# Kernel tuning notes

Measured on AMD Instinct MI355X. Metric: run time of the kernel, lower is better.

The kernel has to match this reference:

```python
import jax, jax.numpy as jnp
import numpy as np

DEPTH, FEAT, HID = 20, 2048, 1024
HALF = FEAT // 2
CLAMP = 2.0
TWO_OVER_PI = 0.6366197723675814  # FrEIA's 0.636619772


def setup_inputs() -> dict:
    key = jax.random.key(0)
    ks = jax.random.split(key, 9)
    x = jax.random.normal(ks[0], (4096, FEAT), dtype=jnp.float32)
    # FrEIA PermuteRandom: numpy permutation seeded with layer index k
    perms = jnp.asarray(
        np.stack([np.random.RandomState(k).permutation(FEAT) for k in range(DEPTH)]),
        dtype=jnp.int32,
    )
    def w(k, shape):  # module reinits all params as 0.01*randn
        return 0.01 * jax.random.normal(k, shape, dtype=jnp.float32)
    return {
        "x": x, "perms": perms,
        "s1_w1": w(ks[1], (DEPTH, HALF, HID)), "s1_b1": w(ks[2], (DEPTH, HID)),
        "s1_w2": w(ks[3], (DEPTH, HID, FEAT)), "s1_b2": w(ks[4], (DEPTH, FEAT)),
        "s2_w1": w(ks[5], (DEPTH, HALF, HID)), "s2_b1": w(ks[6], (DEPTH, HID)),
        "s2_w2": w(ks[7], (DEPTH, HID, FEAT)), "s2_b2": w(ks[8], (DEPTH, FEAT)),
    }


def _subnet(x, w1, b1, w2, b2):
    h = x @ w1 + b1
    h = jnp.where(h >= 0, h, 0.01 * h)  # LeakyReLU(negative_slope=0.01)
    return h @ w2 + b2


def reference(x, perms, s1_w1, s1_b1, s1_w2, s1_b2, s2_w1, s2_b1, s2_w2, s2_b2):
    def body(carry, xs):
        z, jac = carry
        perm, w1a, b1a, w1b, b1b, w2a, b2a, w2b, b2b = xs
        z = z[:, perm]                       # PermuteRandom
        x1, x2 = z[:, :HALF], z[:, HALF:]    # GLOW coupling split
        r2 = _subnet(x2, w2a, b2a, w2b, b2b)  # [B, FEAT] -> (s2, t2)
        e2 = CLAMP * TWO_OVER_PI * jnp.arctan(r2[:, :HALF] / CLAMP)
        y1 = jnp.exp(e2) * x1 + r2[:, HALF:]
        r1 = _subnet(y1, w1a, b1a, w1b, b1b)  # (s1, t1)
        e1 = CLAMP * TWO_OVER_PI * jnp.arctan(r1[:, :HALF] / CLAMP)
        y2 = jnp.exp(e1) * x2 + r1[:, HALF:]
        jac = jac + e1.sum(-1) + e2.sum(-1)  # log|det J| per sample
        return (jnp.concatenate([y1, y2], axis=-1), jac), None

    jac0 = jnp.zeros(x.shape[0], dtype=x.dtype)
    (z, jac), _ = jax.lax.scan(
        body, (x, jac0),
        (perms, s1_w1, s1_b1, s1_w2, s1_b2, s2_w1, s2_b1, s2_w2, s2_b2),
    )
    return z, jac
```

## Files before the change

kernel.cpp:

```cpp
#include <hip/hip_runtime.h>
#include <stdint.h>

#define DEPTH 20
#define FEAT  2048
#define HALF  1024
#define HID   1024
#define MROWS 4096

typedef __bf16 bf16x8 __attribute__((ext_vector_type(8)));
typedef float  f32x4  __attribute__((ext_vector_type(4)));
typedef unsigned int u32x4 __attribute__((ext_vector_type(4)));

__device__ __forceinline__ unsigned short f2bf(float f) {
  union { float f; unsigned int u; } v; v.f = f;
  unsigned int u = v.u + 0x7fffu + ((v.u >> 16) & 1u);
  return (unsigned short)(u >> 16);
}

__device__ __forceinline__ void async_cp16(unsigned short* lds, const unsigned short* g) {
  __builtin_amdgcn_global_load_lds(
      (const __attribute__((address_space(1))) void*)g,
      (__attribute__((address_space(3))) void*)lds, 16, 0, 0);
}

__device__ __forceinline__ bf16x8 lds_ld8(const unsigned short* p) {
  return __builtin_bit_cast(bf16x8, *(const u32x4*)p);
}

__global__ void wcvt_k(const float* __restrict__ s2w1, const float* __restrict__ s2w2,
                       const float* __restrict__ s1w1, const float* __restrict__ s1w2,
                       unsigned short* __restrict__ w2a, unsigned short* __restrict__ w2b,
                       unsigned short* __restrict__ w1a, unsigned short* __restrict__ w1b) {
  const float* src; unsigned short* dst; int N, pp;
  switch (blockIdx.z) {
    case 0:  src = s2w1; dst = w2a; N = 1024; pp = 0; break;
    case 1:  src = s2w2; dst = w2b; N = 2048; pp = 1; break;
    case 2:  src = s1w1; dst = w1a; N = 1024; pp = 0; break;
    default: src = s1w2; dst = w1b; N = 2048; pp = 1; break;
  }
  int nb = blockIdx.x * 32;
  if (nb >= N) return;
  int kb = blockIdx.y * 32;
  __shared__ float t[32][33];
  int tx = threadIdx.x, ty = threadIdx.y;
#pragma unroll
  for (int s = 0; s < 4; ++s)
    t[ty + 8*s][tx] = src[(size_t)(kb + ty + 8*s) * N + nb + tx];
  __syncthreads();
  int pbase = pp ? (nb < 1024 ? 2*nb : 2*(nb - 1024) + 32) : nb;
#pragma unroll
  for (int s = 0; s < 4; ++s) {
    int nl = ty + 8*s;
    dst[(size_t)(pbase + nl) * 1024 + kb + tx] = f2bf(t[tx][nl]);
  }
}

__device__ __forceinline__ int porig(int p) {
  int g = p >> 6, o = p & 63;
  return (o < 32) ? (g*32 + o) : (1024 + g*32 + (o - 32));
}

__global__ void bias_k(const float* __restrict__ s2b1, const float* __restrict__ s2b2,
                       const float* __restrict__ s1b1, const float* __restrict__ s1b2,
                       float* __restrict__ b2a, float* __restrict__ b2b,
                       float* __restrict__ b1a, float* __restrict__ b1b) {
  int i = blockIdx.x * 256 + threadIdx.x;
  if (i < 1024)      b2a[i] = s2b1[i];
  else if (i < 3072) { int p = i - 1024; b2b[p] = s2b2[porig(p)]; }
  else if (i < 4096) b1a[i - 3072] = s1b1[i - 3072];
  else               { int p = i - 4096; b1b[p] = s1b2[porig(p)]; }
}

__global__ void permute_k(const float* __restrict__ z, const int* __restrict__ perm,
                          float* __restrict__ x1f, float* __restrict__ x2f,
                          unsigned short* __restrict__ x2b) {
  int c = blockIdx.x * 256 + threadIdx.x;
  int row0 = blockIdx.y * 8;
  int pc = perm[c];
#pragma unroll
  for (int r = 0; r < 8; ++r) {
    int row = row0 + r;
    float v = z[row * FEAT + pc];
    if (c < HALF) {
      x1f[row * HALF + c] = v;
    } else {
      x2f[row * HALF + c - HALF] = v;
      x2b[row * HALF + c - HALF] = f2bf(v);
    }
  }
}

template<int EPI>
__launch_bounds__(256)
__global__ void gemm_k(const unsigned short* __restrict__ A,
                       const unsigned short* __restrict__ Bt,
                       const float* __restrict__ bias,
                       const float* __restrict__ xin,
                       float* __restrict__ yout,
                       unsigned short* __restrict__ ybf,
                       float* __restrict__ jac,
                       unsigned short* __restrict__ hout) {
  __shared__ unsigned short As[128 * 32];
  __shared__ unsigned short Bs[128 * 32];
  const int tid  = threadIdx.x;
  const int wave = tid >> 6, lane = tid & 63;
  const int quad = lane >> 4, l15 = lane & 15;
  const int wy = wave >> 1, wx = wave & 1;
  const int bm = blockIdx.y * 128;
  const int bn = blockIdx.x * 128;
  const int K = 1024;

  f32x4 acc[4][4];
#pragma unroll
  for (int i = 0; i < 4; ++i)
#pragma unroll
    for (int j = 0; j < 4; ++j)
#pragma unroll
      for (int r = 0; r < 4; ++r) acc[i][j][r] = 0.0f;

  const int gbase = wave * 64 + lane;

  for (int kt = 0; kt < 32; ++kt) {
    const int k0 = kt * 32;
#pragma unroll
    for (int i = 0; i < 2; ++i) {
      int g  = i * 256 + gbase;
      int r  = g >> 2, kg = g & 3;
      async_cp16(&As[(i * 256 + wave * 64) * 8], A  + (size_t)(bm + r) * K + k0 + kg * 8);
      async_cp16(&Bs[(i * 256 + wave * 64) * 8], Bt + (size_t)(bn + r) * K + k0 + kg * 8);
    }
    asm volatile("s_waitcnt vmcnt(0)" ::: "memory");
    __syncthreads();

    bf16x8 af[4], bf[4];
#pragma unroll
    for (int i = 0; i < 4; ++i)
      af[i] = lds_ld8(&As[(wy * 64 + i * 16 + l15) * 32 + quad * 8]);
#pragma unroll
    for (int j = 0; j < 4; ++j)
      bf[j] = lds_ld8(&Bs[(wx * 64 + j * 16 + l15) * 32 + quad * 8]);
#pragma unroll
    for (int i = 0; i < 4; ++i)
#pragma unroll
      for (int j = 0; j < 4; ++j)
        acc[i][j] = __builtin_amdgcn_mfma_f32_16x16x32_bf16(af[i], bf[j], acc[i][j], 0, 0, 0);
    __syncthreads();
  }

  if (EPI == 0) {
    const int ldo = gridDim.x * 128;
#pragma unroll
    for (int j = 0; j < 4; ++j) {
      int col = bn + wx * 64 + j * 16 + l15;
      float bj = bias[col];
#pragma unroll
      for (int i = 0; i < 4; ++i) {
#pragma unroll
        for (int r = 0; r < 4; ++r) {
          int row = bm + wy * 64 + i * 16 + quad * 4 + r;
          float v = acc[i][j][r] + bj;
          v = v >= 0.0f ? v : 0.01f * v;
          hout[(size_t)row * ldo + col] = f2bf(v);
        }
      }
    }
  } else {
    const int g = (bn >> 6) + wx;
#pragma unroll
    for (int i = 0; i < 4; ++i) {
      float esum[4] = {0.0f, 0.0f, 0.0f, 0.0f};
#pragma unroll
      for (int j = 0; j < 2; ++j) {
        int pe = bn + wx * 64 + j * 16 + l15;
        float be = bias[pe];
        float ba = bias[pe + 32];
        int xcol = g * 32 + j * 16 + l15;
#pragma unroll
        for (int r = 0; r < 4; ++r) {
          int row = bm + wy * 64 + i * 16 + quad * 4 + r;
          float re = acc[i][j][r] + be;
          float ra = acc[i][j + 2][r] + ba;
          float e  = 1.2732395447351628f * atanf(0.5f * re);
          float y  = __expf(e) * xin[(size_t)row * HALF + xcol] + ra;
          yout[(size_t)row * FEAT + xcol] = y;
          if (ybf) ybf[(size_t)row * HALF + xcol] = f2bf(y);
          esum[r] += e;
        }
      }
#pragma unroll
      for (int r = 0; r < 4; ++r) {
        float v = esum[r];
        v += __shfl_xor(v, 1);
        v += __shfl_xor(v, 2);
        v += __shfl_xor(v, 4);
        v += __shfl_xor(v, 8);
        if (l15 == 0) {
          int row = bm + wy * 64 + i * 16 + quad * 4 + r;
          atomicAdd(&jac[row], v);
        }
      }
    }
  }
}

__global__ void jcopy_k(const float* __restrict__ jac, float* __restrict__ out) {
  int i = blockIdx.x * 256 + threadIdx.x;
  if (i < 4096) out[i] = jac[i];
}

extern "C" void kernel_launch(void* const* d_in, const int* in_sizes, int n_in,
                              void* d_out, int out_size, void* d_ws, size_t ws_size,
                              hipStream_t stream) {
  const float* x     = (const float*)d_in[0];
  const int*   perms = (const int*)d_in[1];
  const float* s1w1  = (const float*)d_in[2];
  const float* s1b1  = (const float*)d_in[3];
  const float* s1w2  = (const float*)d_in[4];
  const float* s1b2  = (const float*)d_in[5];
  const float* s2w1  = (const float*)d_in[6];
  const float* s2b1  = (const float*)d_in[7];
  const float* s2w2  = (const float*)d_in[8];
  const float* s2b2  = (const float*)d_in[9];
  float* out = (float*)d_out;

  size_t off = 0;
  char* base = (char*)d_ws;
  auto alloc = [&](size_t bytes) {
    void* r = base + off;
    off += (bytes + 255) & ~(size_t)255;
    return r;
  };
  float*          x1f = (float*)alloc((size_t)MROWS * HALF * 4);
  float*          x2f = (float*)alloc((size_t)MROWS * HALF * 4);
  unsigned short* x2b = (unsigned short*)alloc((size_t)MROWS * HALF * 2);
  unsigned short* y1b = (unsigned short*)alloc((size_t)MROWS * HALF * 2);
  unsigned short* hb  = (unsigned short*)alloc((size_t)MROWS * HID * 2);
  float*          zbuf= (float*)alloc((size_t)MROWS * FEAT * 4);
  unsigned short* w2a = (unsigned short*)alloc((size_t)HALF * HID * 2);
  unsigned short* w2b = (unsigned short*)alloc((size_t)FEAT * HID * 2);
  unsigned short* w1a = (unsigned short*)alloc((size_t)HALF * HID * 2);
  unsigned short* w1b = (unsigned short*)alloc((size_t)FEAT * HID * 2);
  float* b2a = (float*)alloc(1024 * 4);
  float* b2b = (float*)alloc(2048 * 4);
  float* b1a = (float*)alloc(1024 * 4);
  float* b1b = (float*)alloc(2048 * 4);
  float* jac = (float*)alloc(4096 * 4);

  hipMemsetAsync(jac, 0, 4096 * 4, stream);

  for (int d = 0; d < DEPTH; ++d) {
    wcvt_k<<<dim3(64, 32, 4), dim3(32, 8), 0, stream>>>(
        s2w1 + (size_t)d * HALF * HID, s2w2 + (size_t)d * HID * FEAT,
        s1w1 + (size_t)d * HALF * HID, s1w2 + (size_t)d * HID * FEAT,
        w2a, w2b, w1a, w1b);
    bias_k<<<24, 256, 0, stream>>>(s2b1 + (size_t)d * HID, s2b2 + (size_t)d * FEAT,
                                   s1b1 + (size_t)d * HID, s1b2 + (size_t)d * FEAT,
                                   b2a, b2b, b1a, b1b);
    const float* zsrc = (d == 0) ? x : zbuf;
    permute_k<<<dim3(8, 512), 256, 0, stream>>>(zsrc, perms + (size_t)d * FEAT, x1f, x2f, x2b);

    float* zdst = (d == DEPTH - 1) ? out : zbuf;
    gemm_k<0><<<dim3(8, 32), 256, 0, stream>>>(x2b, w2a, b2a, nullptr, nullptr, nullptr, nullptr, hb);
    gemm_k<1><<<dim3(16, 32), 256, 0, stream>>>(hb, w2b, b2b, x1f, zdst, y1b, jac, nullptr);
    gemm_k<0><<<dim3(8, 32), 256, 0, stream>>>(y1b, w1a, b1a, nullptr, nullptr, nullptr, nullptr, hb);
    gemm_k<1><<<dim3(16, 32), 256, 0, stream>>>(hb, w1b, b1b, x2f, zdst + HALF, nullptr, jac, nullptr);
  }
  jcopy_k<<<16, 256, 0, stream>>>(jac, out + (size_t)MROWS * FEAT);
}
```

Measured before the change: 3.763 ms.

## Triple-buffer GEMM LDS tiles and hoist weight conversion out of layer loop

The GEMM main loop now uses three LDS buffers with asynchronous global-to-LDS loads issued two k-tiles ahead, waiting only on older loads via partial vmcnt counts. This overlaps memory latency with MFMA work where the old loop serialized load, wait, and compute. Separately, weight transposition/bf16 conversion and bias reordering for all layers are done in one batched launch before the loop, removing 40 small launches. The cost is three times the LDS per block, which may reduce occupancy, plus more workspace for all-layer bf16 weights.

```diff
diff --git a/kernel.cpp b/kernel.cpp
--- a/kernel.cpp
+++ b/kernel.cpp
@@ -27,16 +27,24 @@
   return __builtin_bit_cast(bf16x8, *(const u32x4*)p);
 }
 
+__device__ __forceinline__ void wg_barrier() {
+  asm volatile("" ::: "memory");
+  __builtin_amdgcn_s_barrier();
+  asm volatile("" ::: "memory");
+}
+
 __global__ void wcvt_k(const float* __restrict__ s2w1, const float* __restrict__ s2w2,
                        const float* __restrict__ s1w1, const float* __restrict__ s1w2,
                        unsigned short* __restrict__ w2a, unsigned short* __restrict__ w2b,
                        unsigned short* __restrict__ w1a, unsigned short* __restrict__ w1b) {
+  const int zid = blockIdx.z;
+  const int d = zid >> 2, which = zid & 3;
   const float* src; unsigned short* dst; int N, pp;
-  switch (blockIdx.z) {
-    case 0:  src = s2w1; dst = w2a; N = 1024; pp = 0; break;
-    case 1:  src = s2w2; dst = w2b; N = 2048; pp = 1; break;
-    case 2:  src = s1w1; dst = w1a; N = 1024; pp = 0; break;
-    default: src = s1w2; dst = w1b; N = 2048; pp = 1; break;
+  switch (which) {
+    case 0:  src = s2w1 + (size_t)d * HALF * HID;  dst = w2a + (size_t)d * HALF * HID; N = 1024; pp = 0; break;
+    case 1:  src = s2w2 + (size_t)d * HID * FEAT;  dst = w2b + (size_t)d * FEAT * HID; N = 2048; pp = 1; break;
+    case 2:  src = s1w1 + (size_t)d * HALF * HID;  dst = w1a + (size_t)d * HALF * HID; N = 1024; pp = 0; break;
+    default: src = s1w2 + (size_t)d * HID * FEAT;  dst = w1b + (size_t)d * FEAT * HID; N = 2048; pp = 1; break;
   }
   int nb = blockIdx.x * 32;
   if (nb >= N) return;
@@ -65,10 +73,12 @@
                        float* __restrict__ b2a, float* __restrict__ b2b,
                        float* __restrict__ b1a, float* __restrict__ b1b) {
   int i = blockIdx.x * 256 + threadIdx.x;
-  if (i < 1024)      b2a[i] = s2b1[i];
-  else if (i < 3072) { int p = i - 1024; b2b[p] = s2b2[porig(p)]; }
-  else if (i < 4096) b1a[i - 3072] = s1b1[i - 3072];
-  else               { int p = i - 4096; b1b[p] = s1b2[porig(p)]; }
+  if (i >= DEPTH * 6144) return;
+  int d = i / 6144, j = i - d * 6144;
+  if (j < 1024)      b2a[d*1024 + j] = s2b1[(size_t)d*HID + j];
+  else if (j < 3072) { int p = j - 1024; b2b[d*2048 + p] = s2b2[(size_t)d*FEAT + porig(p)]; }
+  else if (j < 4096) b1a[d*1024 + j - 3072] = s1b1[(size_t)d*HID + j - 3072];
+  else               { int p = j - 4096; b1b[d*2048 + p] = s1b2[(size_t)d*FEAT + porig(p)]; }
 }
 
 __global__ void permute_k(const float* __restrict__ z, const int* __restrict__ perm,
@@ -100,8 +110,8 @@
                        unsigned short* __restrict__ ybf,
                        float* __restrict__ jac,
                        unsigned short* __restrict__ hout) {
-  __shared__ unsigned short As[128 * 32];
-  __shared__ unsigned short Bs[128 * 32];
+  __shared__ unsigned short As[3][128 * 32];
+  __shared__ unsigned short Bs[3][128 * 32];
   const int tid  = threadIdx.x;
   const int wave = tid >> 6, lane = tid & 63;
   const int quad = lane >> 4, l15 = lane & 15;
@@ -120,31 +130,47 @@
 
   const int gbase = wave * 64 + lane;
 
-  for (int kt = 0; kt < 32; ++kt) {
+  auto stage = [&](int kt, int buf) {
     const int k0 = kt * 32;
 #pragma unroll
     for (int i = 0; i < 2; ++i) {
       int g  = i * 256 + gbase;
       int r  = g >> 2, kg = g & 3;
-      async_cp16(&As[(i * 256 + wave * 64) * 8], A  + (size_t)(bm + r) * K + k0 + kg * 8);
-      async_cp16(&Bs[(i * 256 + wave * 64) * 8], Bt + (size_t)(bn + r) * K + k0 + kg * 8);
-    }
-    asm volatile("s_waitcnt vmcnt(0)" ::: "memory");
-    __syncthreads();
+      async_cp16(&As[buf][(i * 256 + wave * 64) * 8], A  + (size_t)(bm + r) * K + k0 + kg * 8);
+      async_cp16(&Bs[buf][(i * 256 + wave * 64) * 8], Bt + (size_t)(bn + r) * K + k0 + kg * 8);
+    }
+  };
+
+  stage(0, 0);
+  stage(1, 1);
+
+  int cb = 0;
+  for (int kt = 0; kt < 32; ++kt) {
+    if (kt < 30) {
+      stage(kt + 2, (kt + 2) % 3);
+      asm volatile("s_waitcnt vmcnt(8)" ::: "memory");
+    } else if (kt == 30) {
+      asm volatile("s_waitcnt vmcnt(4)" ::: "memory");
+    } else {
+      asm volatile("s_waitcnt vmcnt(0)" ::: "memory");
+    }
+    wg_barrier();
 
     bf16x8 af[4], bf[4];
 #pragma unroll
     for (int i = 0; i < 4; ++i)
-      af[i] = lds_ld8(&As[(wy * 64 + i * 16 + l15) * 32 + quad * 8]);
+      af[i] = lds_ld8(&As[cb][(wy * 64 + i * 16 + l15) * 32 + quad * 8]);
 #pragma unroll
     for (int j = 0; j < 4; ++j)
-      bf[j] = lds_ld8(&Bs[(wx * 64 + j * 16 + l15) * 32 + quad * 8]);
+      bf[j] = lds_ld8(&Bs[cb][(wx * 64 + j * 16 + l15) * 32 + quad * 8]);
 #pragma unroll
     for (int i = 0; i < 4; ++i)
 #pragma unroll
       for (int j = 0; j < 4; ++j)
         acc[i][j] = __builtin_amdgcn_mfma_f32_16x16x32_bf16(af[i], bf[j], acc[i][j], 0, 0, 0);
-    __syncthreads();
+
+    wg_barrier();
+    cb = (cb == 2) ? 0 : cb + 1;
   }
 
   if (EPI == 0) {
@@ -236,34 +262,41 @@
   unsigned short* y1b = (unsigned short*)alloc((size_t)MROWS * HALF * 2);
   unsigned short* hb  = (unsigned short*)alloc((size_t)MROWS * HID * 2);
   float*          zbuf= (float*)alloc((size_t)MROWS * FEAT * 4);
-  unsigned short* w2a = (unsigned short*)alloc((size_t)HALF * HID * 2);
-  unsigned short* w2b = (unsigned short*)alloc((size_t)FEAT * HID * 2);
-  unsigned short* w1a = (unsigned short*)alloc((size_t)HALF * HID * 2);
-  unsigned short* w1b = (unsigned short*)alloc((size_t)FEAT * HID * 2);
-  float* b2a = (float*)alloc(1024 * 4);
-  float* b2b = (float*)alloc(2048 * 4);
-  float* b1a = (float*)alloc(1024 * 4);
-  float* b1b = (float*)alloc(2048 * 4);
+  unsigned short* w2a = (unsigned short*)alloc((size_t)DEPTH * HALF * HID * 2);
+  unsigned short* w2b = (unsigned short*)alloc((size_t)DEPTH * FEAT * HID * 2);
+  unsigned short* w1a = (unsigned short*)alloc((size_t)DEPTH * HALF * HID * 2);
+  unsigned short* w1b = (unsigned short*)alloc((size_t)DEPTH * FEAT * HID * 2);
+  float* b2a = (float*)alloc((size_t)DEPTH * 1024 * 4);
+  float* b2b = (float*)alloc((size_t)DEPTH * 2048 * 4);
+  float* b1a = (float*)alloc((size_t)DEPTH * 1024 * 4);
+  float* b1b = (float*)alloc((size_t)DEPTH * 2048 * 4);
   float* jac = (float*)alloc(4096 * 4);
 
   hipMemsetAsync(jac, 0, 4096 * 4, stream);
 
+  wcvt_k<<<dim3(64, 32, 4 * DEPTH), dim3(32, 8), 0, stream>>>(
+      s2w1, s2w2, s1w1, s1w2, w2a, w2b, w1a, w1b);
+  bias_k<<<(DEPTH * 6144 + 255) / 256, 256, 0, stream>>>(
+      s2b1, s2b2, s1b1, s1b2, b2a, b2b, b1a, b1b);
+
   for (int d = 0; d < DEPTH; ++d) {
-    wcvt_k<<<dim3(64, 32, 4), dim3(32, 8), 0, stream>>>(
-        s2w1 + (size_t)d * HALF * HID, s2w2 + (size_t)d * HID * FEAT,
-        s1w1 + (size_t)d * HALF * HID, s1w2 + (size_t)d * HID * FEAT,
-        w2a, w2b, w1a, w1b);
-    bias_k<<<24, 256, 0, stream>>>(s2b1 + (size_t)d * HID, s2b2 + (size_t)d * FEAT,
-                                   s1b1 + (size_t)d * HID, s1b2 + (size_t)d * FEAT,
-                                   b2a, b2b, b1a, b1b);
     const float* zsrc = (d == 0) ? x : zbuf;
     permute_k<<<dim3(8, 512), 256, 0, stream>>>(zsrc, perms + (size_t)d * FEAT, x1f, x2f, x2b);
 
+    unsigned short* W2a = w2a + (size_t)d * HALF * HID;
+    unsigned short* W2b = w2b + (size_t)d * FEAT * HID;
+    unsigned short* W1a = w1a + (size_t)d * HALF * HID;
+    unsigned short* W1b = w1b + (size_t)d * FEAT * HID;
+    float* B2a = b2a + (size_t)d * 1024;
+    float* B2b = b2b + (size_t)d * 2048;
+    float* B1a = b1a + (size_t)d * 1024;
+    float* B1b = b1b + (size_t)d * 2048;
+
     float* zdst = (d == DEPTH - 1) ? out : zbuf;
-    gemm_k<0><<<dim3(8, 32), 256, 0, stream>>>(x2b, w2a, b2a, nullptr, nullptr, nullptr, nullptr, hb);
-    gemm_k<1><<<dim3(16, 32), 256, 0, stream>>>(hb, w2b, b2b, x1f, zdst, y1b, jac, nullptr);
-    gemm_k<0><<<dim3(8, 32), 256, 0, stream>>>(y1b, w1a, b1a, nullptr, nullptr, nullptr, nullptr, hb);
-    gemm_k<1><<<dim3(16, 32), 256, 0, stream>>>(hb, w1b, b1b, x2f, zdst + HALF, nullptr, jac, nullptr);
+    gemm_k<0><<<dim3(8, 32), 256, 0, stream>>>(x2b, W2a, B2a, nullptr, nullptr, nullptr, nullptr, hb);
+    gemm_k<1><<<dim3(16, 32), 256, 0, stream>>>(hb, W2b, B2b, x1f, zdst, y1b, jac, nullptr);
+    gemm_k<0><<<dim3(8, 32), 256, 0, stream>>>(y1b, W1a, B1a, nullptr, nullptr, nullptr, nullptr, hb);
+    gemm_k<1><<<dim3(16, 32), 256, 0, stream>>>(hb, W1b, B1b, x2f, zdst + HALF, nullptr, jac, nullptr);
   }
   jcopy_k<<<16, 256, 0, stream>>>(jac, out + (size_t)MROWS * FEAT);
 }
```

After: 4.081 ms. 1.08x slower.
